# Performance work log

Hardware: AMD Instinct MI355X
Metric: run time of the kernel (lower is better)

The kernel has to match this reference:

```python
import jax, jax.numpy as jnp
import numpy as np

N_CHAN = 64
N_PTS = 2048
D_IN = 256
D_OUT = 256
N_FRAMES = 32  # config.n_frames; no_frames = N_FRAMES - 1


def setup_inputs() -> dict:
    key = jax.random.key(0)
    k1, k2, k3, k4, k5 = jax.random.split(key, 5)
    x = jax.random.normal(k1, (N_CHAN, N_PTS, D_IN), dtype=jnp.float32)
    t = jax.random.uniform(k2, (1, N_CHAN, 1), dtype=jnp.float32)
    model_idx = jax.random.randint(k3, (N_CHAN,), 0, N_CHAN)
    # per-channel weights, SIREN-style uniform init scale
    bound = 1.0 / np.sqrt(D_IN)
    W = jax.random.uniform(k4, (N_CHAN, D_IN, D_OUT), minval=-bound, maxval=bound, dtype=jnp.float32)
    B = jax.random.uniform(k5, (N_FRAMES, D_OUT), minval=-bound, maxval=bound, dtype=jnp.float32)
    return {"x": x, "t": t, "model_idx": model_idx, "W": W, "B": B}


def reference(x, t, model_idx, W, B):
    no_frames = N_FRAMES - 1
    # bias index per channel from the time coordinate: (t[0,:,0] * no_frames).long()
    bias_idx = (t[0, :, 0] * no_frames).astype(jnp.int32)  # [C]
    Wg = W[model_idx]          # [C, D_IN, D_OUT] gathered per-channel weights
    bg = B[bias_idx]           # [C, D_OUT] gathered per-channel biases
    # batched per-channel linear: x [C, N, D_IN] @ Wg [C, D_IN, D_OUT]
    out = jnp.einsum('cni,cio->cno', x, Wg) + bg[:, None, :]
    return out
```

## Files before the change

kernel.cpp:

```cpp
#include <hip/hip_runtime.h>
#include <hip/hip_bf16.h>


#define M_PTS 2048
#define K_DIM 256
#define N_DIM 256
#define BT_STRIDE 264

typedef float floatx4 __attribute__((ext_vector_type(4)));
typedef __bf16 bf16x4 __attribute__((ext_vector_type(4)));
typedef __bf16 bf16x8 __attribute__((ext_vector_type(8)));

__device__ __forceinline__ __bf16 cvt_bf16(float f) {
  unsigned u = __builtin_bit_cast(unsigned, f);
  unsigned r = (u + 0x7FFFu + ((u >> 16) & 1u)) >> 16;
  return __builtin_bit_cast(__bf16, (unsigned short)r);
}

__global__ __launch_bounds__(256) void fused_k(
    const float* __restrict__ X, const float* __restrict__ T,
    const int* __restrict__ MI, const float* __restrict__ W,
    const float* __restrict__ Bb, float* __restrict__ Out) {
  __shared__ __bf16 As[128 * 32];
  __shared__ __bf16 Bt[128 * BT_STRIDE];

  const int bid = blockIdx.x;
  const int c   = bid >> 4;
  const int mg  = (bid >> 1) & 7;
  const int nt  = bid & 1;
  const int n0  = nt * 128;

  const float* __restrict__ Xc = X + (size_t)c * (M_PTS * K_DIM);
  const float* __restrict__ Wc = W + (size_t)MI[c] * (K_DIM * N_DIM);

  const int tid  = threadIdx.x;
  const int lane = tid & 63;
  const int w    = tid >> 6;
  const int wm   = w & 1;
  const int wn   = w >> 1;
  const int r    = lane & 15;
  const int kg   = lane >> 4;

  {
    const int n  = tid & 127;
    const int kq = tid >> 7;
    const float* __restrict__ src = Wc + (size_t)(kq * 128) * N_DIM + n0 + n;
    __bf16* __restrict__ dst = &Bt[n * BT_STRIDE + kq * 128];
#pragma unroll 4
    for (int u = 0; u < 32; ++u) {
      bf16x4 v;
      v.x = cvt_bf16(src[(size_t)(u * 4 + 0) * N_DIM]);
      v.y = cvt_bf16(src[(size_t)(u * 4 + 1) * N_DIM]);
      v.z = cvt_bf16(src[(size_t)(u * 4 + 2) * N_DIM]);
      v.w = cvt_bf16(src[(size_t)(u * 4 + 3) * N_DIM]);
      *(bf16x4*)&dst[u * 4] = v;
    }
  }

  const int sm  = tid >> 1;
  const int skh = (tid & 1) * 16;
  const float* __restrict__ xrow = Xc + skh;
  __bf16* __restrict__ adst = &As[sm * 32 + skh];

  int bidx = (int)(T[c] * 31.0f);
  bidx = bidx < 0 ? 0 : (bidx > 31 ? 31 : bidx);
  const float* __restrict__ brow = Bb + bidx * N_DIM + n0 + wn * 64;
  float bv[4];
#pragma unroll
  for (int j = 0; j < 4; ++j) bv[j] = brow[j * 16 + r];

  float* __restrict__ Oc = Out + (size_t)c * (M_PTS * N_DIM);

  for (int mt2 = 0; mt2 < 2; ++mt2) {
    const int m0 = mg * 256 + mt2 * 128;
    const float* __restrict__ xsrc = xrow + (size_t)(m0 + sm) * K_DIM;
    floatx4 acc[4][4] = {};

    for (int kt = 0; kt < 8; ++kt) {
      const int k0 = kt * 32;
      __syncthreads();
      {
        floatx4 f0 = *(const floatx4*)(xsrc + k0 + 0);
        floatx4 f1 = *(const floatx4*)(xsrc + k0 + 4);
        floatx4 f2 = *(const floatx4*)(xsrc + k0 + 8);
        floatx4 f3 = *(const floatx4*)(xsrc + k0 + 12);
        bf16x8 h0, h1;
#pragma unroll
        for (int v = 0; v < 4; ++v) {
          h0[v]     = cvt_bf16(f0[v]);
          h0[v + 4] = cvt_bf16(f1[v]);
          h1[v]     = cvt_bf16(f2[v]);
          h1[v + 4] = cvt_bf16(f3[v]);
        }
        *(bf16x8*)&adst[0] = h0;
        *(bf16x8*)&adst[8] = h1;
      }
      __syncthreads();

      bf16x8 a[4], b[4];
#pragma unroll
      for (int i = 0; i < 4; ++i)
        a[i] = *(const bf16x8*)&As[(wm * 64 + i * 16 + r) * 32 + kg * 8];
#pragma unroll
      for (int j = 0; j < 4; ++j)
        b[j] = *(const bf16x8*)&Bt[(wn * 64 + j * 16 + r) * BT_STRIDE + k0 + kg * 8];
#pragma unroll
      for (int i = 0; i < 4; ++i)
#pragma unroll
        for (int j = 0; j < 4; ++j)
          acc[i][j] = __builtin_amdgcn_mfma_f32_16x16x32_bf16(a[i], b[j], acc[i][j], 0, 0, 0);
    }

#pragma unroll
    for (int i = 0; i < 4; ++i) {
#pragma unroll
      for (int j = 0; j < 4; ++j) {
        const int col = n0 + wn * 64 + j * 16 + r;
#pragma unroll
        for (int v = 0; v < 4; ++v) {
          const int row = m0 + wm * 64 + i * 16 + kg * 4 + v;
          Oc[(size_t)row * N_DIM + col] = acc[i][j][v] + bv[j];
        }
      }
    }
  }
}

extern "C" void kernel_launch(void* const* d_in, const int* in_sizes, int n_in,
                              void* d_out, int out_size, void* d_ws, size_t ws_size,
                              hipStream_t stream) {
  const float* X   = (const float*)d_in[0];
  const float* T   = (const float*)d_in[1];
  const int* MI    = (const int*)d_in[2];
  const float* W   = (const float*)d_in[3];
  const float* Bb  = (const float*)d_in[4];
  float* Out       = (float*)d_out;

  fused_k<<<dim3(1024), dim3(256), 0, stream>>>(X, T, MI, W, Bb, Out);
}
```

Measured before the change: 272.3 us.

## Split into weight pre-transpose kernel and LDS-free direct-load bf16 GEMM

Adds a pre-pass kernel that gathers each channel's weight matrix, transposes it and converts it to bf16 in the workspace. A new GEMM kernel then loads X and the pre-transposed weights directly from global memory into MFMA operands without shared memory or barriers, using 128x128 tiles across 2048 blocks. This removes the per-block strided weight conversion that the fused kernel repeated, at the cost of an extra launch, a workspace round trip, and register-based global loads that may be less coalesced. The old fused kernel remains as a fallback when no workspace is available.

```diff
diff --git a/kernel.cpp b/kernel.cpp
--- a/kernel.cpp
+++ b/kernel.cpp
@@ -1,11 +1,11 @@
 #include <hip/hip_runtime.h>
-#include <hip/hip_bf16.h>
 
 
 #define M_PTS 2048
 #define K_DIM 256
 #define N_DIM 256
 #define BT_STRIDE 264
+#define WT_BYTES ((size_t)64 * K_DIM * N_DIM * 2)
 
 typedef float floatx4 __attribute__((ext_vector_type(4)));
 typedef __bf16 bf16x4 __attribute__((ext_vector_type(4)));
@@ -15,6 +15,117 @@
   unsigned u = __builtin_bit_cast(unsigned, f);
   unsigned r = (u + 0x7FFFu + ((u >> 16) & 1u)) >> 16;
   return __builtin_bit_cast(__bf16, (unsigned short)r);
+}
+
+__global__ __launch_bounds__(256) void wt_k(const float* __restrict__ W,
+                                            const int* __restrict__ MI,
+                                            __bf16* __restrict__ Wt) {
+  __shared__ float tile[64][65];
+  const int bid = blockIdx.x;
+  const int c  = bid >> 4;
+  const int kt = (bid >> 2) & 3;
+  const int nt = bid & 3;
+  const float* __restrict__ src =
+      W + (size_t)MI[c] * (K_DIM * N_DIM) + (size_t)(kt * 64) * N_DIM + nt * 64;
+  __bf16* __restrict__ dst =
+      Wt + (size_t)c * (K_DIM * N_DIM) + (size_t)(nt * 64) * K_DIM + kt * 64;
+  const int tid = threadIdx.x;
+  {
+    const int nl = tid & 63, kl0 = tid >> 6;
+#pragma unroll
+    for (int u = 0; u < 16; ++u)
+      tile[kl0 + u * 4][nl] = src[(size_t)(kl0 + u * 4) * N_DIM + nl];
+  }
+  __syncthreads();
+  {
+    const int kl = tid & 63, nl0 = tid >> 6;
+#pragma unroll
+    for (int u = 0; u < 16; ++u)
+      dst[(size_t)(nl0 + u * 4) * K_DIM + kl] = cvt_bf16(tile[kl][nl0 + u * 4]);
+  }
+}
+
+__global__ __launch_bounds__(256) void gemm_k(const float* __restrict__ X,
+                                              const float* __restrict__ T,
+                                              const __bf16* __restrict__ Wt,
+                                              const float* __restrict__ Bb,
+                                              float* __restrict__ Out) {
+  const int bid = blockIdx.x;
+  const int c   = bid >> 5;
+  const int mg  = (bid >> 1) & 15;
+  const int nt  = bid & 1;
+  const int n0  = nt * 128;
+  const int m0  = mg * 128;
+
+  const int tid  = threadIdx.x;
+  const int lane = tid & 63;
+  const int w    = tid >> 6;
+  const int wm   = w & 1;
+  const int wn   = w >> 1;
+  const int r    = lane & 15;
+  const int kg   = lane >> 4;
+
+  const float*  __restrict__ Xc = X  + (size_t)c * (M_PTS * K_DIM);
+  const __bf16* __restrict__ Wc = Wt + (size_t)c * (K_DIM * N_DIM);
+
+  const float* xa[4];
+  const __bf16* wb[4];
+#pragma unroll
+  for (int i = 0; i < 4; ++i)
+    xa[i] = Xc + (size_t)(m0 + wm * 64 + i * 16 + r) * K_DIM + kg * 8;
+#pragma unroll
+  for (int j = 0; j < 4; ++j)
+    wb[j] = Wc + (size_t)(n0 + wn * 64 + j * 16 + r) * K_DIM + kg * 8;
+
+  int bidx = (int)(T[c] * 31.0f);
+  bidx = bidx < 0 ? 0 : (bidx > 31 ? 31 : bidx);
+  const float* __restrict__ brow = Bb + bidx * N_DIM + n0 + wn * 64;
+  float bv[4];
+#pragma unroll
+  for (int j = 0; j < 4; ++j) bv[j] = brow[j * 16 + r];
+
+  floatx4 acc[4][4] = {};
+
+#pragma unroll 2
+  for (int kt = 0; kt < 8; ++kt) {
+    const int k0 = kt * 32;
+    floatx4 f0[4], f1[4];
+    bf16x8 b[4];
+#pragma unroll
+    for (int i = 0; i < 4; ++i) {
+      f0[i] = *(const floatx4*)(xa[i] + k0);
+      f1[i] = *(const floatx4*)(xa[i] + k0 + 4);
+    }
+#pragma unroll
+    for (int j = 0; j < 4; ++j) b[j] = *(const bf16x8*)(wb[j] + k0);
+    bf16x8 a[4];
+#pragma unroll
+    for (int i = 0; i < 4; ++i)
+#pragma unroll
+      for (int v = 0; v < 4; ++v) {
+        a[i][v]     = cvt_bf16(f0[i][v]);
+        a[i][v + 4] = cvt_bf16(f1[i][v]);
+      }
+#pragma unroll
+    for (int i = 0; i < 4; ++i)
+#pragma unroll
+      for (int j = 0; j < 4; ++j)
+        acc[i][j] = __builtin_amdgcn_mfma_f32_16x16x32_bf16(a[i], b[j], acc[i][j], 0, 0, 0);
+  }
+
+  float* __restrict__ Oc = Out + (size_t)c * (M_PTS * N_DIM);
+#pragma unroll
+  for (int i = 0; i < 4; ++i) {
+#pragma unroll
+    for (int j = 0; j < 4; ++j) {
+      const int col = n0 + wn * 64 + j * 16 + r;
+#pragma unroll
+      for (int v = 0; v < 4; ++v) {
+        const int row = m0 + wm * 64 + i * 16 + kg * 4 + v;
+        Oc[(size_t)row * N_DIM + col] = acc[i][j][v] + bv[j];
+      }
+    }
+  }
 }
 
 __global__ __launch_bounds__(256) void fused_k(
@@ -136,5 +247,11 @@
   const float* Bb  = (const float*)d_in[4];
   float* Out       = (float*)d_out;
 
-  fused_k<<<dim3(1024), dim3(256), 0, stream>>>(X, T, MI, W, Bb, Out);
-}
+  if (ws_size >= WT_BYTES && d_ws != nullptr) {
+    __bf16* Wt = (__bf16*)d_ws;
+    wt_k<<<dim3(1024), dim3(256), 0, stream>>>(W, MI, Wt);
+    gemm_k<<<dim3(2048), dim3(256), 0, stream>>>(X, T, Wt, Bb, Out);
+  } else {
+    fused_k<<<dim3(1024), dim3(256), 0, stream>>>(X, T, MI, W, Bb, Out);
+  }
+}
```

New measurement: 304.6 us. 1.12x slower.
